# Optimization experiments

Hardware: AMD Instinct MI355X
Metric: run time of the kernel (lower is better)

Reference implementation:

```python
import jax, jax.numpy as jnp
import numpy as np

N = 50000        # nodes
E = 1_600_000    # edges
IN = 64          # in_channels
HID = 16         # hidden_dim (per-head channels)
HEADS = 8
OUT = 32         # out_channels
B = 256          # graphs in batch
NEG_SLOPE = 0.2  # PyG GATv2Conv default


def gatv2_conv(x, edge_index, wl, bl, wr, br, att, bias, heads, ch, concat, num_nodes):
    """Faithful GATv2Conv (PyG semantics, eval mode, add self-loops disabled upstream
    is not the case in PyG default, but the module uses default add_self_loops=True;
    we add them here)."""
    src, dst = edge_index[0], edge_index[1]
    # PyG default add_self_loops=True
    loop = jnp.arange(num_nodes, dtype=src.dtype)
    src = jnp.concatenate([src, loop])
    dst = jnp.concatenate([dst, loop])
    xl = (x @ wl + bl).reshape(num_nodes, heads, ch)  # source transform
    xr = (x @ wr + br).reshape(num_nodes, heads, ch)  # target transform
    # per-edge GATv2 score: att . leaky_relu(xl[src] + xr[dst])
    e = jax.nn.leaky_relu(xl[src] + xr[dst], NEG_SLOPE)          # [E, H, C]
    logits = jnp.einsum('ehc,hc->eh', e, att)                     # [E, H]
    # segment softmax over incoming edges of each dst node (max detached, as in PyG)
    m = jax.lax.stop_gradient(jax.ops.segment_max(logits, dst, num_segments=num_nodes))
    a = jnp.exp(logits - m[dst])
    denom = jax.ops.segment_sum(a, dst, num_segments=num_nodes)
    alpha = a / (denom[dst] + 1e-16)                              # [E, H]
    msg = xl[src] * alpha[..., None]                              # [E, H, C]
    out = jax.ops.segment_sum(msg, dst, num_segments=num_nodes)   # [N, H, C]
    if concat:
        out = out.reshape(num_nodes, heads * ch) + bias
    else:
        out = out.mean(axis=1) + bias
    return out


def global_mean_pool(x, batch, num_graphs):
    s = jax.ops.segment_sum(x, batch, num_segments=num_graphs)
    cnt = jax.ops.segment_sum(jnp.ones((x.shape[0],), x.dtype), batch, num_segments=num_graphs)
    return s / jnp.maximum(cnt, 1.0)[:, None]


def setup_inputs() -> dict:
    key = jax.random.key(0)
    ks = jax.random.split(key, 24)
    f32 = jnp.float32
    def g(k, shape, s=0.1):
        return jax.random.normal(k, shape, f32) * s
    inp = {
        'x': jax.random.normal(ks[0], (N, IN), f32),
        'edge_index': jax.random.randint(ks[1], (2, E), 0, N, dtype=jnp.int32),
        'batch': jnp.sort(jax.random.randint(ks[2], (N,), 0, B, dtype=jnp.int32)),
        # conv1: GATv2Conv(IN -> HID, heads=HEADS, concat=True)
        'wl1': g(ks[3], (IN, HEADS * HID)), 'bl1': jnp.zeros((HEADS * HID,), f32),
        'wr1': g(ks[4], (IN, HEADS * HID)), 'br1': jnp.zeros((HEADS * HID,), f32),
        'att1': g(ks[5], (HEADS, HID)),
        'bias1': jnp.zeros((HEADS * HID,), f32),
        # conv2: GATv2Conv(HEADS*HID -> HID, heads=1, concat=False)
        'wl2': g(ks[6], (HEADS * HID, HID)), 'bl2': jnp.zeros((HID,), f32),
        'wr2': g(ks[7], (HEADS * HID, HID)), 'br2': jnp.zeros((HID,), f32),
        'att2': g(ks[8], (1, HID)),
        'bias2': jnp.zeros((HID,), f32),
        # MLP: HID -> 2*HID -> HID -> OUT
        'w_m1': g(ks[9], (HID, 2 * HID)), 'b_m1': jnp.zeros((2 * HID,), f32),
        'w_m2': g(ks[10], (2 * HID, HID)), 'b_m2': jnp.zeros((HID,), f32),
        'w_m3': g(ks[11], (HID, OUT)), 'b_m3': jnp.zeros((OUT,), f32),
    }
    return inp


def reference(x, edge_index, batch,
              wl1, bl1, wr1, br1, att1, bias1,
              wl2, bl2, wr2, br2, att2, bias2,
              w_m1, b_m1, w_m2, b_m2, w_m3, b_m3):
    # eval mode: all dropouts are identity
    h = jax.nn.elu(gatv2_conv(x, edge_index, wl1, bl1, wr1, br1, att1, bias1,
                              HEADS, HID, True, N))
    h = jax.nn.elu(gatv2_conv(h, edge_index, wl2, bl2, wr2, br2, att2, bias2,
                              1, HID, False, N))
    h = global_mean_pool(h, batch, B)                 # [B, HID]
    h = jax.nn.elu(h @ w_m1 + b_m1)
    h = jax.nn.elu(h @ w_m2 + b_m2)
    return h @ w_m3 + b_m3                            # [B, OUT]
```

## Files before the change

### kernel.cpp

```cpp
#include <hip/hip_runtime.h>
#include <hip/hip_bf16.h>
#include <hip/hip_fp16.h>
#include <math.h>

#define NN   50000
#define NE   1600000
#define EP   (NE + NN)
#define NB   256
#define BK_SH 6
#define BKN  (1 << BK_SH)
#define NBKT ((NN + BKN - 1) >> BK_SH)
#define CAP_SH 12
#define CAP  (1 << CAP_SH)
#define ET   8
#define EB   (256 * ET)
#define EBLK ((NE + EB - 1) / EB)
#define G1   ((NN + 31) / 32)

__device__ __forceinline__ float elu_f(float x)   { return x > 0.0f ? x : expm1f(x); }
__device__ __forceinline__ float lrelu_f(float x) { return fmaxf(x, 0.2f * x); }

typedef _Float16 f16x2 __attribute__((ext_vector_type(2)));

__global__ __launch_bounds__(256) void k_gemm1_bucket(
    const float* __restrict__ x, const float* __restrict__ wl,
    const float* __restrict__ bl, const float* __restrict__ wr,
    const float* __restrict__ br, __half* __restrict__ xl1, float* __restrict__ xr1,
    const int* __restrict__ ei, int* __restrict__ bcursor,
    unsigned int* __restrict__ bb)
{
    __shared__ float xs[32 * 64];
    __shared__ int lh[NBKT];
    __shared__ int cur[NBKT];
    const int tid = threadIdx.x;

    if (blockIdx.x < G1) {
        const int n0  = blockIdx.x * 32;
        const int nrem = min(32, NN - n0);

        const float4* xg = (const float4*)(x + (size_t)n0 * 64);
        float4* xs4 = (float4*)xs;
        const int lim4 = nrem * 16;
        for (int i = tid; i < lim4; i += 256) xs4[i] = xg[i];
        __syncthreads();

        const int g  = tid >> 6;
        const int c0 = (tid & 63) * 4;
        const bool isl = (c0 < 128);
        const float* w  = isl ? wl : wr;
        const float* b  = isl ? bl : br;
        const int    cw = isl ? c0 : (c0 - 128);

        float4 acc[8];
#pragma unroll
        for (int r = 0; r < 8; ++r) acc[r] = make_float4(0.f, 0.f, 0.f, 0.f);

        for (int k4 = 0; k4 < 16; ++k4) {
            const float4 w0 = *(const float4*)&w[(k4*4+0)*128 + cw];
            const float4 w1 = *(const float4*)&w[(k4*4+1)*128 + cw];
            const float4 w2 = *(const float4*)&w[(k4*4+2)*128 + cw];
            const float4 w3 = *(const float4*)&w[(k4*4+3)*128 + cw];
#pragma unroll
            for (int r = 0; r < 8; ++r) {
                const float4 xv = xs4[(g*8+r)*16 + k4];
                acc[r].x += xv.x*w0.x + xv.y*w1.x + xv.z*w2.x + xv.w*w3.x;
                acc[r].y += xv.x*w0.y + xv.y*w1.y + xv.z*w2.y + xv.w*w3.y;
                acc[r].z += xv.x*w0.z + xv.y*w1.z + xv.z*w2.z + xv.w*w3.z;
                acc[r].w += xv.x*w0.w + xv.y*w1.w + xv.z*w2.w + xv.w*w3.w;
            }
        }
        const float4 bv = *(const float4*)&b[cw];
#pragma unroll
        for (int r = 0; r < 8; ++r) {
            const int row = g*8 + r;
            if (row < nrem) {
                float4 o = make_float4(acc[r].x + bv.x, acc[r].y + bv.y,
                                       acc[r].z + bv.z, acc[r].w + bv.w);
                if (isl) {
                    __half2* dst = (__half2*)&xl1[(size_t)(n0 + row) * 128 + cw];
                    dst[0] = __floats2half2_rn(o.x, o.y);
                    dst[1] = __floats2half2_rn(o.z, o.w);
                } else {
                    *(float4*)&xr1[(size_t)(n0 + row) * 128 + cw] = o;
                }
            }
        }
    } else {
        const int bid = blockIdx.x - G1;
        for (int i = tid; i < NBKT; i += 256) lh[i] = 0;
        __syncthreads();

        const int t = bid * 256 + tid;
        const bool act = (t * ET < NE);
        int4 dreg[ET / 4];
        if (act) {
            const int4* dp = (const int4*)&ei[NE + t * ET];
#pragma unroll
            for (int q = 0; q < ET / 4; ++q) {
                dreg[q] = dp[q];
                atomicAdd(&lh[dreg[q].x >> BK_SH], 1);
                atomicAdd(&lh[dreg[q].y >> BK_SH], 1);
                atomicAdd(&lh[dreg[q].z >> BK_SH], 1);
                atomicAdd(&lh[dreg[q].w >> BK_SH], 1);
            }
        }
        __syncthreads();
        for (int i = tid; i < NBKT; i += 256) {
            int h = lh[i];
            if (h > 0) cur[i] = (i << CAP_SH) + atomicAdd(&bcursor[i], h);
        }
        __syncthreads();
        if (act) {
            const int4* sp = (const int4*)&ei[t * ET];
#pragma unroll
            for (int q = 0; q < ET / 4; ++q) {
                int4 s = sp[q];
                int4 d = dreg[q];
                int bkt, p;
                bkt = d.x >> BK_SH; p = atomicAdd(&cur[bkt], 1);
                if (p < ((bkt + 1) << CAP_SH))
                    bb[p] = ((unsigned)(d.x & (BKN-1)) << 17) | (unsigned)s.x;
                bkt = d.y >> BK_SH; p = atomicAdd(&cur[bkt], 1);
                if (p < ((bkt + 1) << CAP_SH))
                    bb[p] = ((unsigned)(d.y & (BKN-1)) << 17) | (unsigned)s.y;
                bkt = d.z >> BK_SH; p = atomicAdd(&cur[bkt], 1);
                if (p < ((bkt + 1) << CAP_SH))
                    bb[p] = ((unsigned)(d.z & (BKN-1)) << 17) | (unsigned)s.z;
                bkt = d.w >> BK_SH; p = atomicAdd(&cur[bkt], 1);
                if (p < ((bkt + 1) << CAP_SH))
                    bb[p] = ((unsigned)(d.w & (BKN-1)) << 17) | (unsigned)s.w;
            }
        }
    }
}

__global__ __launch_bounds__(256) void k_bfinal(
    const unsigned int* __restrict__ bb, const int* __restrict__ bcursor,
    int* __restrict__ rowp, int* __restrict__ slist)
{
    __shared__ int cnt[BKN], cur[BKN];
    __shared__ int red[256];
    const int b = blockIdx.x, tid = threadIdx.x;
    const int db0 = b << BK_SH;
    const int dn  = min(BKN, NN - db0);

    int part = 0;
    for (int i = tid; i < b; i += 256)
        part += min(bcursor[i], CAP);
    red[tid] = part;
    __syncthreads();
    for (int ofs = 128; ofs >= 1; ofs >>= 1) {
        if (tid < ofs) red[tid] += red[tid + ofs];
        __syncthreads();
    }
    const int ebeg = red[0];
    const int count = min(bcursor[b], CAP);
    const unsigned int* src = bb + ((size_t)b << CAP_SH);
    const int out0 = ebeg + db0;

    int c0 = 0;
    if (tid < BKN) {
        c0 = (tid < dn) ? 1 : 0;
        cnt[tid] = c0;
    }
    __syncthreads();
    for (int i = tid; i < count; i += 256)
        atomicAdd(&cnt[src[i] >> 17], 1);
    __syncthreads();
    if (tid < BKN) c0 = cnt[tid];
    for (int ofs = 1; ofs < BKN; ofs <<= 1) {
        int v = 0;
        if (tid < BKN && tid >= ofs) v = cnt[tid - ofs];
        __syncthreads();
        if (tid < BKN) cnt[tid] += v;
        __syncthreads();
    }
    if (tid < BKN) {
        int ex = cnt[tid] - c0;
        cur[tid] = ex + 1;
        if (tid < dn) {
            rowp[db0 + tid] = out0 + ex;
            slist[out0 + ex] = db0 + tid;
        }
    }
    if (b == 0 && tid == 0) rowp[NN] = EP;
    __syncthreads();
    for (int i = tid; i < count; i += 256) {
        unsigned u = src[i];
        int p = atomicAdd(&cur[u >> 17], 1);
        slist[out0 + p] = (int)(u & 0x1FFFFu);
    }
}

__global__ __launch_bounds__(256) void k_conv1_agg(
    const __half* __restrict__ xl1, const float* __restrict__ xr1,
    const float* __restrict__ att, const float* __restrict__ bias1,
    const int* __restrict__ rowp, const int* __restrict__ slist,
    const float* __restrict__ wl2, const float* __restrict__ bl2,
    const float* __restrict__ wr2, const float* __restrict__ br2,
    __half* __restrict__ xl2, float* __restrict__ xr2)
{
    __shared__ float wcombt[32 * 132];
    __shared__ float bcomb[32];
    __shared__ float h1rows[4 * 128];
    const int tid = threadIdx.x;

    for (int i = tid; i < 2048; i += 256) {
        const int cc = i >> 4, jj = i & 15;
        wcombt[jj * 132 + cc]        = wl2[i];
        wcombt[(16 + jj) * 132 + cc] = wr2[i];
    }
    if (tid < 16) { bcomb[tid] = bl2[tid]; bcomb[16 + tid] = br2[tid]; }

    const int d = (blockIdx.x * 256 + tid) >> 6;
    const int lane = tid & 63;
    const int h = lane >> 3, e = lane & 7;
    const int cb = h * 16;

    f16x2 xrh[8], ath[8];
    {
        const float4* xrp = (const float4*)&xr1[(size_t)d * 128 + cb];
        const float4* atp = (const float4*)&att[cb];
#pragma unroll
        for (int q = 0; q < 4; ++q) {
            float4 a4 = xrp[q];
            xrh[2*q]   = (f16x2){(_Float16)a4.x, (_Float16)a4.y};
            xrh[2*q+1] = (f16x2){(_Float16)a4.z, (_Float16)a4.w};
            float4 b4 = atp[q];
            ath[2*q]   = (f16x2){(_Float16)b4.x, (_Float16)b4.y};
            ath[2*q+1] = (f16x2){(_Float16)b4.z, (_Float16)b4.w};
        }
    }
    const f16x2 c02 = {(_Float16)0.2f, (_Float16)0.2f};

    const int beg = rowp[d], end = rowp[d + 1];

    float den = 0.f;
    float a[16];
#pragma unroll
    for (int c = 0; c < 16; ++c) a[c] = 0.f;

    for (int base = beg; base < end; base += 64) {
        const int nb = min(64, end - base);
        int sv = (lane < nb) ? slist[base + lane] : 0;
        for (int c8 = 0; c8 * 8 < nb; c8 += 2) {
            const int idx0 = c8 * 8 + e;
            const int idx1 = idx0 + 8;
            const int s0 = __shfl(sv, idx0);
            const int s1 = __shfl(sv, idx1 & 63);
            const bool e0 = (idx0 < nb), e1 = (idx1 < nb);
            float4 p0, p1, q0, q1;
            if (e0) {
                const float4* vp = (const float4*)(xl1 + (size_t)s0 * 128 + cb);
                p0 = vp[0]; p1 = vp[1];
            }
            if (e1) {
                const float4* vp = (const float4*)(xl1 + (size_t)s1 * 128 + cb);
                q0 = vp[0]; q1 = vp[1];
            }
            if (e0) {
                const f16x2* hh = (const f16x2*)&p0;
                const f16x2* hg = (const f16x2*)&p1;
                float s = 0.f;
#pragma unroll
                for (int q = 0; q < 4; ++q) {
                    f16x2 t = hh[q] + xrh[q];
                    t = __builtin_elementwise_max(t, t * c02);
                    s = __builtin_amdgcn_fdot2(ath[q], t, s, false);
                }
#pragma unroll
                for (int q = 0; q < 4; ++q) {
                    f16x2 t = hg[q] + xrh[4+q];
                    t = __builtin_elementwise_max(t, t * c02);
                    s = __builtin_amdgcn_fdot2(ath[4+q], t, s, false);
                }
                const float w = __expf(fminf(s, 80.f));
                den += w;
#pragma unroll
                for (int q = 0; q < 4; ++q) {
                    a[2*q]     += w * (float)hh[q].x;
                    a[2*q+1]   += w * (float)hh[q].y;
                    a[8+2*q]   += w * (float)hg[q].x;
                    a[8+2*q+1] += w * (float)hg[q].y;
                }
            }
            if (e1) {
                const f16x2* hh = (const f16x2*)&q0;
                const f16x2* hg = (const f16x2*)&q1;
                float s = 0.f;
#pragma unroll
                for (int q = 0; q < 4; ++q) {
                    f16x2 t = hh[q] + xrh[q];
                    t = __builtin_elementwise_max(t, t * c02);
                    s = __builtin_amdgcn_fdot2(ath[q], t, s, false);
                }
#pragma unroll
                for (int q = 0; q < 4; ++q) {
                    f16x2 t = hg[q] + xrh[4+q];
                    t = __builtin_elementwise_max(t, t * c02);
                    s = __builtin_amdgcn_fdot2(ath[4+q], t, s, false);
                }
                const float w = __expf(fminf(s, 80.f));
                den += w;
#pragma unroll
                for (int q = 0; q < 4; ++q) {
                    a[2*q]     += w * (float)hh[q].x;
                    a[2*q+1]   += w * (float)hh[q].y;
                    a[8+2*q]   += w * (float)hg[q].x;
                    a[8+2*q+1] += w * (float)hg[q].y;
                }
            }
        }
    }

    den += __shfl_xor(den, 1);
    den += __shfl_xor(den, 2);
    den += __shfl_xor(den, 4);

    const bool b0 = (e & 1), b1 = (e & 2), b2 = (e & 4);
    float t1[8], u1[8];
#pragma unroll
    for (int j = 0; j < 8; ++j) {
        t1[j] = b0 ? a[j + 8] : a[j];
        u1[j] = b0 ? a[j] : a[j + 8];
    }
#pragma unroll
    for (int j = 0; j < 8; ++j) t1[j] += __shfl_xor(u1[j], 1);
    float t2[4], u2[4];
#pragma unroll
    for (int j = 0; j < 4; ++j) {
        t2[j] = b1 ? t1[j + 4] : t1[j];
        u2[j] = b1 ? t1[j] : t1[j + 4];
    }
#pragma unroll
    for (int j = 0; j < 4; ++j) t2[j] += __shfl_xor(u2[j], 2);
    float t3[2], u3[2];
#pragma unroll
    for (int j = 0; j < 2; ++j) {
        t3[j] = b2 ? t2[j + 2] : t2[j];
        u3[j] = b2 ? t2[j] : t2[j + 2];
    }
#pragma unroll
    for (int j = 0; j < 2; ++j) t3[j] += __shfl_xor(u3[j], 4);

    const int c0 = (b0 ? 8 : 0) + (b1 ? 4 : 0) + (b2 ? 2 : 0);
    const float inv = 1.0f / (den + 1e-16f);
    const int c = cb + c0;
    const float o0 = elu_f(t3[0] * inv + bias1[c]);
    const float o1 = elu_f(t3[1] * inv + bias1[c + 1]);

    const int wv = tid >> 6;
    *(float2*)&h1rows[wv * 128 + c] = make_float2(o0, o1);
    __syncthreads();
    {
        const int j = lane & 31;
        const int half = lane >> 5;
        const float* hr = &h1rows[wv * 128 + half * 64];
        const float* wc = &wcombt[j * 132 + half * 64];
        float sum = 0.f;
#pragma unroll
        for (int cc = 0; cc < 64; cc += 4) {
            const float4 hv = *(const float4*)&hr[cc];
            const float4 wv4 = *(const float4*)&wc[cc];
            sum += hv.x*wv4.x + hv.y*wv4.y + hv.z*wv4.z + hv.w*wv4.w;
        }
        sum += __shfl_xor(sum, 32);
        if (half == 0) {
            sum += bcomb[j];
            if (j < 16) xl2[(size_t)d * 16 + j] = __float2half(sum);
            else        xr2[(size_t)d * 16 + (j - 16)] = sum;
        }
    }
}

__global__ __launch_bounds__(256) void k_conv2_agg(
    const __half* __restrict__ xl2, const float* __restrict__ xr2,
    const float* __restrict__ att, const float* __restrict__ bias2,
    const int* __restrict__ rowp, const int* __restrict__ slist,
    float* __restrict__ h2)
{
    const int d = (blockIdx.x * 256 + threadIdx.x) >> 6;
    if (d >= NN) return;
    const int lane = threadIdx.x & 63;

    f16x2 xrh[8], ath[8];
    {
        const float4* xrp = (const float4*)&xr2[(size_t)d * 16];
        const float4* atp = (const float4*)&att[0];
#pragma unroll
        for (int q = 0; q < 4; ++q) {
            float4 a4 = xrp[q];
            xrh[2*q]   = (f16x2){(_Float16)a4.x, (_Float16)a4.y};
            xrh[2*q+1] = (f16x2){(_Float16)a4.z, (_Float16)a4.w};
            float4 b4 = atp[q];
            ath[2*q]   = (f16x2){(_Float16)b4.x, (_Float16)b4.y};
            ath[2*q+1] = (f16x2){(_Float16)b4.z, (_Float16)b4.w};
        }
    }
    const f16x2 c02 = {(_Float16)0.2f, (_Float16)0.2f};

    const int beg = rowp[d];
    const int total = rowp[d + 1] - beg;

    float den = 0.f;
    float a[16];
#pragma unroll
    for (int c = 0; c < 16; ++c) a[c] = 0.f;

    for (int j = lane; j < total; j += 64) {
        const int src = slist[beg + j];
        const float4* vp = (const float4*)(xl2 + (size_t)src * 16);
        const float4 r0 = vp[0], r1 = vp[1];
        const f16x2* hh = (const f16x2*)&r0;
        const f16x2* hg = (const f16x2*)&r1;
        float s = 0.f;
#pragma unroll
        for (int q = 0; q < 4; ++q) {
            f16x2 t = hh[q] + xrh[q];
            t = __builtin_elementwise_max(t, t * c02);
            s = __builtin_amdgcn_fdot2(ath[q], t, s, false);
        }
#pragma unroll
        for (int q = 0; q < 4; ++q) {
            f16x2 t = hg[q] + xrh[4+q];
            t = __builtin_elementwise_max(t, t * c02);
            s = __builtin_amdgcn_fdot2(ath[4+q], t, s, false);
        }
        const float w = __expf(fminf(s, 80.f));
        den += w;
#pragma unroll
        for (int q = 0; q < 4; ++q) {
            a[2*q]     += w * (float)hh[q].x;
            a[2*q+1]   += w * (float)hh[q].y;
            a[8+2*q]   += w * (float)hg[q].x;
            a[8+2*q+1] += w * (float)hg[q].y;
        }
    }

    den += __shfl_xor(den, 1);
    den += __shfl_xor(den, 2);
    den += __shfl_xor(den, 4);
    den += __shfl_xor(den, 8);
    den += __shfl_xor(den, 16);
    den += __shfl_xor(den, 32);

    const bool b0 = (lane & 1), b1 = (lane & 2), b2 = (lane & 4), b3 = (lane & 8);
    float t1[8], u1[8];
#pragma unroll
    for (int j = 0; j < 8; ++j) {
        t1[j] = b0 ? a[j + 8] : a[j];
        u1[j] = b0 ? a[j] : a[j + 8];
    }
#pragma unroll
    for (int j = 0; j < 8; ++j) t1[j] += __shfl_xor(u1[j], 1);
    float t2[4], u2[4];
#pragma unroll
    for (int j = 0; j < 4; ++j) {
        t2[j] = b1 ? t1[j + 4] : t1[j];
        u2[j] = b1 ? t1[j] : t1[j + 4];
    }
#pragma unroll
    for (int j = 0; j < 4; ++j) t2[j] += __shfl_xor(u2[j], 2);
    float t3[2], u3[2];
#pragma unroll
    for (int j = 0; j < 2; ++j) {
        t3[j] = b2 ? t2[j + 2] : t2[j];
        u3[j] = b2 ? t2[j] : t2[j + 2];
    }
#pragma unroll
    for (int j = 0; j < 2; ++j) t3[j] += __shfl_xor(u3[j], 4);
    float t4 = b3 ? t3[1] : t3[0];
    float u4 = b3 ? t3[0] : t3[1];
    t4 += __shfl_xor(u4, 8);
    t4 += __shfl_xor(t4, 16);
    t4 += __shfl_xor(t4, 32);

    if (lane < 16) {
        const int c = (b0 ? 8 : 0) + (b1 ? 4 : 0) + (b2 ? 2 : 0) + (b3 ? 1 : 0);
        const float inv = 1.0f / (den + 1e-16f);
        h2[(size_t)d * 16 + c] = elu_f(t4 * inv + bias2[c]);
    }
}

__global__ __launch_bounds__(256) void k_pool_mlp(
    const float* __restrict__ h2, const int* __restrict__ batch,
    const float* __restrict__ w1, const float* __restrict__ b1,
    const float* __restrict__ w2, const float* __restrict__ b2,
    const float* __restrict__ w3, const float* __restrict__ b3,
    float* __restrict__ out)
{
    __shared__ int se[2];
    __shared__ float sm[256];
    __shared__ float hb[16], t1s[32], t2s[16];
    const int b = blockIdx.x, tid = threadIdx.x;
    if (tid < 2) {
        int key = b + tid, lo = 0, hi = NN;
        while (lo < hi) {
            int mid = (lo + hi) >> 1;
            if (batch[mid] < key) lo = mid + 1; else hi = mid;
        }
        se[tid] = lo;
    }
    __syncthreads();
    const int s = se[0], e = se[1];
    const int c = tid & 15, slot = tid >> 4;
    float acc = 0.f;
    for (int n = s + slot; n < e; n += 16) acc += h2[(size_t)n * 16 + c];
    sm[tid] = acc;
    __syncthreads();
    for (int ofs = 128; ofs >= 16; ofs >>= 1) {
        if (tid < ofs) sm[tid] += sm[tid + ofs];
        __syncthreads();
    }
    if (tid < 16) hb[tid] = sm[tid] / fmaxf((float)(e - s), 1.0f);
    __syncthreads();
    if (tid < 32) {
        float v = b1[tid];
        for (int k = 0; k < 16; ++k) v += hb[k] * w1[k * 32 + tid];
        t1s[tid] = elu_f(v);
    }
    __syncthreads();
    if (tid < 16) {
        float v = b2[tid];
        for (int k = 0; k < 32; ++k) v += t1s[k] * w2[k * 16 + tid];
        t2s[tid] = elu_f(v);
    }
    __syncthreads();
    if (tid < 32) {
        float v = b3[tid];
        for (int k = 0; k < 16; ++k) v += t2s[k] * w3[k * 32 + tid];
        out[b * 32 + tid] = v;
    }
}

extern "C" void kernel_launch(void* const* d_in, const int* in_sizes, int n_in,
                              void* d_out, int out_size, void* d_ws, size_t ws_size,
                              hipStream_t stream)
{
    const float* x     = (const float*)d_in[0];
    const int*   ei    = (const int*)d_in[1];
    const int*   batch = (const int*)d_in[2];
    const float* wl1   = (const float*)d_in[3];
    const float* bl1   = (const float*)d_in[4];
    const float* wr1   = (const float*)d_in[5];
    const float* br1   = (const float*)d_in[6];
    const float* att1  = (const float*)d_in[7];
    const float* bias1 = (const float*)d_in[8];
    const float* wl2   = (const float*)d_in[9];
    const float* bl2   = (const float*)d_in[10];
    const float* wr2   = (const float*)d_in[11];
    const float* br2   = (const float*)d_in[12];
    const float* att2  = (const float*)d_in[13];
    const float* bias2 = (const float*)d_in[14];
    const float* wm1   = (const float*)d_in[15];
    const float* bm1   = (const float*)d_in[16];
    const float* wm2   = (const float*)d_in[17];
    const float* bm2   = (const float*)d_in[18];
    const float* wm3   = (const float*)d_in[19];
    const float* bm3   = (const float*)d_in[20];
    float* out = (float*)d_out;

    char* base = (char*)d_ws;
    size_t off = 0;
    auto alloc = [&](size_t bytes) -> void* {
        void* p = base + off;
        off += (bytes + 255) & ~(size_t)255;
        return p;
    };
    __half* xl1  = (__half*)alloc((size_t)NN * 128 * 2);
    float* xr1   = (float*)alloc((size_t)NN * 128 * 4);
    int*   slist = (int*)  alloc((size_t)EP * 4);
    unsigned int* bb = (unsigned int*)alloc((size_t)NBKT * CAP * 4);
    int*   rowp  = (int*)  alloc((size_t)(NN + 1) * 4);
    int*   bcursor=(int*)  alloc((size_t)NBKT * 4);
    __half* xl2  = (__half*)alloc((size_t)NN * 16 * 2);
    float* xr2   = (float*)alloc((size_t)NN * 16 * 4);
    float* h2    = (float*)alloc((size_t)NN * 16 * 4);

    (void)hipMemsetAsync(bcursor, 0, (size_t)NBKT * 4, stream);
    k_gemm1_bucket<<<G1 + EBLK, 256, 0, stream>>>(x, wl1, bl1, wr1, br1, xl1, xr1,
                                                  ei, bcursor, bb);
    k_bfinal<<<NBKT, 256, 0, stream>>>(bb, bcursor, rowp, slist);
    k_conv1_agg<<<(NN * 64) / 256, 256, 0, stream>>>(xl1, xr1, att1, bias1, rowp, slist,
                                                     wl2, bl2, wr2, br2, xl2, xr2);
    k_conv2_agg<<<(NN * 64) / 256, 256, 0, stream>>>(xl2, xr2, att2, bias2, rowp, slist, h2);
    k_pool_mlp<<<NB, 256, 0, stream>>>(h2, batch, wm1, bm1, wm2, bm2, wm3, bm3, out);
}
```

Baseline: 279.5 us.

## Fuse CSR bucket finalization into both aggregation kernels via shared-memory local CSR

Removes the separate k_bfinal kernel and the global rowp/slist arrays. Each aggregation block now handles one 64-node bucket with 512 threads, building that bucket's local row pointers and source list in LDS from the bucket buffer, then lets each of 8 waves process 8 destination nodes in turn. This saves one launch and the global CSR write and read-back. In exchange the bucket sort is done twice, once per conv kernel, and the grid is much smaller with a large LDS footprint per block, which can lower occupancy and load balance.

Result: slower. 286.9 us (+2.6%).

```diff
diff --git a/kernel.cpp b/kernel.cpp
--- a/kernel.cpp
+++ b/kernel.cpp
@@ -134,123 +134,105 @@
     }
 }
 
-__global__ __launch_bounds__(256) void k_bfinal(
-    const unsigned int* __restrict__ bb, const int* __restrict__ bcursor,
-    int* __restrict__ rowp, int* __restrict__ slist)
-{
-    __shared__ int cnt[BKN], cur[BKN];
-    __shared__ int red[256];
-    const int b = blockIdx.x, tid = threadIdx.x;
-    const int db0 = b << BK_SH;
-    const int dn  = min(BKN, NN - db0);
-
-    int part = 0;
-    for (int i = tid; i < b; i += 256)
-        part += min(bcursor[i], CAP);
-    red[tid] = part;
-    __syncthreads();
-    for (int ofs = 128; ofs >= 1; ofs >>= 1) {
-        if (tid < ofs) red[tid] += red[tid + ofs];
-        __syncthreads();
-    }
-    const int ebeg = red[0];
-    const int count = min(bcursor[b], CAP);
-    const unsigned int* src = bb + ((size_t)b << CAP_SH);
-    const int out0 = ebeg + db0;
-
-    int c0 = 0;
-    if (tid < BKN) {
-        c0 = (tid < dn) ? 1 : 0;
-        cnt[tid] = c0;
-    }
-    __syncthreads();
-    for (int i = tid; i < count; i += 256)
-        atomicAdd(&cnt[src[i] >> 17], 1);
-    __syncthreads();
-    if (tid < BKN) c0 = cnt[tid];
-    for (int ofs = 1; ofs < BKN; ofs <<= 1) {
-        int v = 0;
-        if (tid < BKN && tid >= ofs) v = cnt[tid - ofs];
-        __syncthreads();
-        if (tid < BKN) cnt[tid] += v;
-        __syncthreads();
-    }
-    if (tid < BKN) {
-        int ex = cnt[tid] - c0;
-        cur[tid] = ex + 1;
-        if (tid < dn) {
-            rowp[db0 + tid] = out0 + ex;
-            slist[out0 + ex] = db0 + tid;
-        }
-    }
-    if (b == 0 && tid == 0) rowp[NN] = EP;
-    __syncthreads();
-    for (int i = tid; i < count; i += 256) {
-        unsigned u = src[i];
-        int p = atomicAdd(&cur[u >> 17], 1);
-        slist[out0 + p] = (int)(u & 0x1FFFFu);
-    }
-}
-
-__global__ __launch_bounds__(256) void k_conv1_agg(
+__global__ __launch_bounds__(512) void k_conv1_agg(
     const __half* __restrict__ xl1, const float* __restrict__ xr1,
     const float* __restrict__ att, const float* __restrict__ bias1,
-    const int* __restrict__ rowp, const int* __restrict__ slist,
+    const unsigned int* __restrict__ bb, const int* __restrict__ bcursor,
     const float* __restrict__ wl2, const float* __restrict__ bl2,
     const float* __restrict__ wr2, const float* __restrict__ br2,
     __half* __restrict__ xl2, float* __restrict__ xr2)
 {
     __shared__ float wcombt[32 * 132];
     __shared__ float bcomb[32];
-    __shared__ float h1rows[4 * 128];
+    __shared__ float h1rows[8 * 128];
+    __shared__ int lcnt[BKN], lcur[BKN];
+    __shared__ int lrowp[BKN + 1];
+    __shared__ int lsl[CAP + BKN];
     const int tid = threadIdx.x;
-
-    for (int i = tid; i < 2048; i += 256) {
+    const int b = blockIdx.x;
+    const int db0 = b << BK_SH;
+    const int dn  = min(BKN, NN - db0);
+    const int count = min(bcursor[b], CAP);
+    const unsigned int* src = bb + ((size_t)b << CAP_SH);
+
+    for (int i = tid; i < 2048; i += 512) {
         const int cc = i >> 4, jj = i & 15;
         wcombt[jj * 132 + cc]        = wl2[i];
         wcombt[(16 + jj) * 132 + cc] = wr2[i];
     }
     if (tid < 16) { bcomb[tid] = bl2[tid]; bcomb[16 + tid] = br2[tid]; }
 
-    const int d = (blockIdx.x * 256 + tid) >> 6;
-    const int lane = tid & 63;
+    int selfc = 0;
+    if (tid < BKN) {
+        selfc = (tid < dn) ? 1 : 0;
+        lcnt[tid] = selfc;
+    }
+    __syncthreads();
+    for (int i = tid; i < count; i += 512)
+        atomicAdd(&lcnt[src[i] >> 17], 1);
+    __syncthreads();
+    int orig = 0;
+    if (tid < BKN) orig = lcnt[tid];
+    for (int ofs = 1; ofs < BKN; ofs <<= 1) {
+        int v = 0;
+        if (tid < BKN && tid >= ofs) v = lcnt[tid - ofs];
+        __syncthreads();
+        if (tid < BKN) lcnt[tid] += v;
+        __syncthreads();
+    }
+    if (tid < BKN) {
+        const int ex = lcnt[tid] - orig;
+        lrowp[tid] = ex;
+        lcur[tid] = ex + 1;
+        if (tid < dn) lsl[ex] = db0 + tid;
+        if (tid == BKN - 1) lrowp[BKN] = lcnt[tid];
+    }
+    __syncthreads();
+    for (int i = tid; i < count; i += 512) {
+        const unsigned u = src[i];
+        const int p = atomicAdd(&lcur[u >> 17], 1);
+        lsl[p] = (int)(u & 0x1FFFFu);
+    }
+    __syncthreads();
+
+    const int wv = tid >> 6, lane = tid & 63;
     const int h = lane >> 3, e = lane & 7;
     const int cb = h * 16;
-
-    f16x2 xrh[8], ath[8];
-    {
-        const float4* xrp = (const float4*)&xr1[(size_t)d * 128 + cb];
-        const float4* atp = (const float4*)&att[cb];
-#pragma unroll
-        for (int q = 0; q < 4; ++q) {
-            float4 a4 = xrp[q];
-            xrh[2*q]   = (f16x2){(_Float16)a4.x, (_Float16)a4.y};
-            xrh[2*q+1] = (f16x2){(_Float16)a4.z, (_Float16)a4.w};
-            float4 b4 = atp[q];
-            ath[2*q]   = (f16x2){(_Float16)b4.x, (_Float16)b4.y};
-            ath[2*q+1] = (f16x2){(_Float16)b4.z, (_Float16)b4.w};
-        }
-    }
     const f16x2 c02 = {(_Float16)0.2f, (_Float16)0.2f};
 
-    const int beg = rowp[d], end = rowp[d + 1];
-
-    float den = 0.f;
-    float a[16];
-#pragma unroll
-    for (int c = 0; c < 16; ++c) a[c] = 0.f;
-
-    for (int base = beg; base < end; base += 64) {
-        const int nb = min(64, end - base);
-        int sv = (lane < nb) ? slist[base + lane] : 0;
-        for (int c8 = 0; c8 * 8 < nb; c8 += 2) {
-            const int idx0 = c8 * 8 + e;
-            const int idx1 = idx0 + 8;
-            const int s0 = __shfl(sv, idx0);
-            const int s1 = __shfl(sv, idx1 & 63);
-            const bool e0 = (idx0 < nb), e1 = (idx1 < nb);
+    for (int di = 0; di < 8; ++di) {
+        const int dloc = wv * 8 + di;
+        if (dloc >= dn) break;
+        const int d = db0 + dloc;
+
+        f16x2 xrh[8], ath[8];
+        {
+            const float4* xrp = (const float4*)&xr1[(size_t)d * 128 + cb];
+            const float4* atp = (const float4*)&att[cb];
+#pragma unroll
+            for (int q = 0; q < 4; ++q) {
+                float4 a4 = xrp[q];
+                xrh[2*q]   = (f16x2){(_Float16)a4.x, (_Float16)a4.y};
+                xrh[2*q+1] = (f16x2){(_Float16)a4.z, (_Float16)a4.w};
+                float4 b4 = atp[q];
+                ath[2*q]   = (f16x2){(_Float16)b4.x, (_Float16)b4.y};
+                ath[2*q+1] = (f16x2){(_Float16)b4.z, (_Float16)b4.w};
+            }
+        }
+        const int beg = lrowp[dloc];
+        const int deg = lrowp[dloc + 1] - beg;
+
+        float den = 0.f;
+        float a[16];
+#pragma unroll
+        for (int c = 0; c < 16; ++c) a[c] = 0.f;
+
+        for (int idx0 = e; idx0 < deg; idx0 += 16) {
+            const int s0 = lsl[beg + idx0];
+            const bool e1 = (idx0 + 8 < deg);
+            const int s1 = e1 ? lsl[beg + idx0 + 8] : 0;
             float4 p0, p1, q0, q1;
-            if (e0) {
+            {
                 const float4* vp = (const float4*)(xl1 + (size_t)s0 * 128 + cb);
                 p0 = vp[0]; p1 = vp[1];
             }
@@ -258,7 +240,7 @@
                 const float4* vp = (const float4*)(xl1 + (size_t)s1 * 128 + cb);
                 q0 = vp[0]; q1 = vp[1];
             }
-            if (e0) {
+            {
                 const f16x2* hh = (const f16x2*)&p0;
                 const f16x2* hg = (const f16x2*)&p1;
                 float s = 0.f;
@@ -311,174 +293,218 @@
                 }
             }
         }
-    }
-
-    den += __shfl_xor(den, 1);
-    den += __shfl_xor(den, 2);
-    den += __shfl_xor(den, 4);
-
-    const bool b0 = (e & 1), b1 = (e & 2), b2 = (e & 4);
-    float t1[8], u1[8];
-#pragma unroll
-    for (int j = 0; j < 8; ++j) {
-        t1[j] = b0 ? a[j + 8] : a[j];
-        u1[j] = b0 ? a[j] : a[j + 8];
-    }
-#pragma unroll
-    for (int j = 0; j < 8; ++j) t1[j] += __shfl_xor(u1[j], 1);
-    float t2[4], u2[4];
-#pragma unroll
-    for (int j = 0; j < 4; ++j) {
-        t2[j] = b1 ? t1[j + 4] : t1[j];
-        u2[j] = b1 ? t1[j] : t1[j + 4];
-    }
-#pragma unroll
-    for (int j = 0; j < 4; ++j) t2[j] += __shfl_xor(u2[j], 2);
-    float t3[2], u3[2];
-#pragma unroll
-    for (int j = 0; j < 2; ++j) {
-        t3[j] = b2 ? t2[j + 2] : t2[j];
-        u3[j] = b2 ? t2[j] : t2[j + 2];
-    }
-#pragma unroll
-    for (int j = 0; j < 2; ++j) t3[j] += __shfl_xor(u3[j], 4);
-
-    const int c0 = (b0 ? 8 : 0) + (b1 ? 4 : 0) + (b2 ? 2 : 0);
-    const float inv = 1.0f / (den + 1e-16f);
-    const int c = cb + c0;
-    const float o0 = elu_f(t3[0] * inv + bias1[c]);
-    const float o1 = elu_f(t3[1] * inv + bias1[c + 1]);
-
-    const int wv = tid >> 6;
-    *(float2*)&h1rows[wv * 128 + c] = make_float2(o0, o1);
-    __syncthreads();
-    {
-        const int j = lane & 31;
-        const int half = lane >> 5;
-        const float* hr = &h1rows[wv * 128 + half * 64];
-        const float* wc = &wcombt[j * 132 + half * 64];
-        float sum = 0.f;
-#pragma unroll
-        for (int cc = 0; cc < 64; cc += 4) {
-            const float4 hv = *(const float4*)&hr[cc];
-            const float4 wv4 = *(const float4*)&wc[cc];
-            sum += hv.x*wv4.x + hv.y*wv4.y + hv.z*wv4.z + hv.w*wv4.w;
-        }
-        sum += __shfl_xor(sum, 32);
-        if (half == 0) {
-            sum += bcomb[j];
-            if (j < 16) xl2[(size_t)d * 16 + j] = __float2half(sum);
-            else        xr2[(size_t)d * 16 + (j - 16)] = sum;
+
+        den += __shfl_xor(den, 1);
+        den += __shfl_xor(den, 2);
+        den += __shfl_xor(den, 4);
+
+        const bool b0 = (e & 1), b1 = (e & 2), b2 = (e & 4);
+        float t1[8], u1[8];
+#pragma unroll
+        for (int j = 0; j < 8; ++j) {
+            t1[j] = b0 ? a[j + 8] : a[j];
+            u1[j] = b0 ? a[j] : a[j + 8];
+        }
+#pragma unroll
+        for (int j = 0; j < 8; ++j) t1[j] += __shfl_xor(u1[j], 1);
+        float t2[4], u2[4];
+#pragma unroll
+        for (int j = 0; j < 4; ++j) {
+            t2[j] = b1 ? t1[j + 4] : t1[j];
+            u2[j] = b1 ? t1[j] : t1[j + 4];
+        }
+#pragma unroll
+        for (int j = 0; j < 4; ++j) t2[j] += __shfl_xor(u2[j], 2);
+        float t3[2], u3[2];
+#pragma unroll
+        for (int j = 0; j < 2; ++j) {
+            t3[j] = b2 ? t2[j + 2] : t2[j];
+            u3[j] = b2 ? t2[j] : t2[j + 2];
+        }
+#pragma unroll
+        for (int j = 0; j < 2; ++j) t3[j] += __shfl_xor(u3[j], 4);
+
+        const int c0 = (b0 ? 8 : 0) + (b1 ? 4 : 0) + (b2 ? 2 : 0);
+        const float inv = 1.0f / (den + 1e-16f);
+        const int c = cb + c0;
+        const float o0 = elu_f(t3[0] * inv + bias1[c]);
+        const float o1 = elu_f(t3[1] * inv + bias1[c + 1]);
+
+        *(float2*)&h1rows[wv * 128 + c] = make_float2(o0, o1);
+        {
+            const int j = lane & 31;
+            const int half = lane >> 5;
+            const float* hr = &h1rows[wv * 128 + half * 64];
+            const float* wc = &wcombt[j * 132 + half * 64];
+            float sum = 0.f;
+#pragma unroll
+            for (int cc = 0; cc < 64; cc += 4) {
+                const float4 hv = *(const float4*)&hr[cc];
+                const float4 wv4 = *(const float4*)&wc[cc];
+                sum += hv.x*wv4.x + hv.y*wv4.y + hv.z*wv4.z + hv.w*wv4.w;
+            }
+            sum += __shfl_xor(sum, 32);
+            if (half == 0) {
+                sum += bcomb[j];
+                if (j < 16) xl2[(size_t)d * 16 + j] = __float2half(sum);
+                else        xr2[(size_t)d * 16 + (j - 16)] = sum;
+            }
         }
     }
 }
 
-__global__ __launch_bounds__(256) void k_conv2_agg(
+__global__ __launch_bounds__(512) void k_conv2_agg(
     const __half* __restrict__ xl2, const float* __restrict__ xr2,
     const float* __restrict__ att, const float* __restrict__ bias2,
-    const int* __restrict__ rowp, const int* __restrict__ slist,
+    const unsigned int* __restrict__ bb, const int* __restrict__ bcursor,
     float* __restrict__ h2)
 {
-    const int d = (blockIdx.x * 256 + threadIdx.x) >> 6;
-    if (d >= NN) return;
-    const int lane = threadIdx.x & 63;
-
-    f16x2 xrh[8], ath[8];
-    {
-        const float4* xrp = (const float4*)&xr2[(size_t)d * 16];
-        const float4* atp = (const float4*)&att[0];
-#pragma unroll
-        for (int q = 0; q < 4; ++q) {
-            float4 a4 = xrp[q];
-            xrh[2*q]   = (f16x2){(_Float16)a4.x, (_Float16)a4.y};
-            xrh[2*q+1] = (f16x2){(_Float16)a4.z, (_Float16)a4.w};
-            float4 b4 = atp[q];
-            ath[2*q]   = (f16x2){(_Float16)b4.x, (_Float16)b4.y};
-            ath[2*q+1] = (f16x2){(_Float16)b4.z, (_Float16)b4.w};
-        }
-    }
+    __shared__ int lcnt[BKN], lcur[BKN];
+    __shared__ int lrowp[BKN + 1];
+    __shared__ int lsl[CAP + BKN];
+    const int tid = threadIdx.x;
+    const int b = blockIdx.x;
+    const int db0 = b << BK_SH;
+    const int dn  = min(BKN, NN - db0);
+    const int count = min(bcursor[b], CAP);
+    const unsigned int* src = bb + ((size_t)b << CAP_SH);
+
+    int selfc = 0;
+    if (tid < BKN) {
+        selfc = (tid < dn) ? 1 : 0;
+        lcnt[tid] = selfc;
+    }
+    __syncthreads();
+    for (int i = tid; i < count; i += 512)
+        atomicAdd(&lcnt[src[i] >> 17], 1);
+    __syncthreads();
+    int orig = 0;
+    if (tid < BKN) orig = lcnt[tid];
+    for (int ofs = 1; ofs < BKN; ofs <<= 1) {
+        int v = 0;
+        if (tid < BKN && tid >= ofs) v = lcnt[tid - ofs];
+        __syncthreads();
+        if (tid < BKN) lcnt[tid] += v;
+        __syncthreads();
+    }
+    if (tid < BKN) {
+        const int ex = lcnt[tid] - orig;
+        lrowp[tid] = ex;
+        lcur[tid] = ex + 1;
+        if (tid < dn) lsl[ex] = db0 + tid;
+        if (tid == BKN - 1) lrowp[BKN] = lcnt[tid];
+    }
+    __syncthreads();
+    for (int i = tid; i < count; i += 512) {
+        const unsigned u = src[i];
+        const int p = atomicAdd(&lcur[u >> 17], 1);
+        lsl[p] = (int)(u & 0x1FFFFu);
+    }
+    __syncthreads();
+
+    const int wv = tid >> 6, lane = tid & 63;
     const f16x2 c02 = {(_Float16)0.2f, (_Float16)0.2f};
 
-    const int beg = rowp[d];
-    const int total = rowp[d + 1] - beg;
-
-    float den = 0.f;
-    float a[16];
-#pragma unroll
-    for (int c = 0; c < 16; ++c) a[c] = 0.f;
-
-    for (int j = lane; j < total; j += 64) {
-        const int src = slist[beg + j];
-        const float4* vp = (const float4*)(xl2 + (size_t)src * 16);
-        const float4 r0 = vp[0], r1 = vp[1];
-        const f16x2* hh = (const f16x2*)&r0;
-        const f16x2* hg = (const f16x2*)&r1;
-        float s = 0.f;
-#pragma unroll
-        for (int q = 0; q < 4; ++q) {
-            f16x2 t = hh[q] + xrh[q];
-            t = __builtin_elementwise_max(t, t * c02);
-            s = __builtin_amdgcn_fdot2(ath[q], t, s, false);
-        }
-#pragma unroll
-        for (int q = 0; q < 4; ++q) {
-            f16x2 t = hg[q] + xrh[4+q];
-            t = __builtin_elementwise_max(t, t * c02);
-            s = __builtin_amdgcn_fdot2(ath[4+q], t, s, false);
-        }
-        const float w = __expf(fminf(s, 80.f));
-        den += w;
-#pragma unroll
-        for (int q = 0; q < 4; ++q) {
-            a[2*q]     += w * (float)hh[q].x;
-            a[2*q+1]   += w * (float)hh[q].y;
-            a[8+2*q]   += w * (float)hg[q].x;
-            a[8+2*q+1] += w * (float)hg[q].y;
-        }
-    }
-
-    den += __shfl_xor(den, 1);
-    den += __shfl_xor(den, 2);
-    den += __shfl_xor(den, 4);
-    den += __shfl_xor(den, 8);
-    den += __shfl_xor(den, 16);
-    den += __shfl_xor(den, 32);
-
-    const bool b0 = (lane & 1), b1 = (lane & 2), b2 = (lane & 4), b3 = (lane & 8);
-    float t1[8], u1[8];
-#pragma unroll
-    for (int j = 0; j < 8; ++j) {
-        t1[j] = b0 ? a[j + 8] : a[j];
-        u1[j] = b0 ? a[j] : a[j + 8];
-    }
-#pragma unroll
-    for (int j = 0; j < 8; ++j) t1[j] += __shfl_xor(u1[j], 1);
-    float t2[4], u2[4];
-#pragma unroll
-    for (int j = 0; j < 4; ++j) {
-        t2[j] = b1 ? t1[j + 4] : t1[j];
-        u2[j] = b1 ? t1[j] : t1[j + 4];
-    }
-#pragma unroll
-    for (int j = 0; j < 4; ++j) t2[j] += __shfl_xor(u2[j], 2);
-    float t3[2], u3[2];
-#pragma unroll
-    for (int j = 0; j < 2; ++j) {
-        t3[j] = b2 ? t2[j + 2] : t2[j];
-        u3[j] = b2 ? t2[j] : t2[j + 2];
-    }
-#pragma unroll
-    for (int j = 0; j < 2; ++j) t3[j] += __shfl_xor(u3[j], 4);
-    float t4 = b3 ? t3[1] : t3[0];
-    float u4 = b3 ? t3[0] : t3[1];
-    t4 += __shfl_xor(u4, 8);
-    t4 += __shfl_xor(t4, 16);
-    t4 += __shfl_xor(t4, 32);
-
-    if (lane < 16) {
-        const int c = (b0 ? 8 : 0) + (b1 ? 4 : 0) + (b2 ? 2 : 0) + (b3 ? 1 : 0);
-        const float inv = 1.0f / (den + 1e-16f);
-        h2[(size_t)d * 16 + c] = elu_f(t4 * inv + bias2[c]);
+    for (int di = 0; di < 8; ++di) {
+        const int dloc = wv * 8 + di;
+        if (dloc >= dn) break;
+        const int d = db0 + dloc;
+
+        f16x2 xrh[8], ath[8];
+        {
+            const float4* xrp = (const float4*)&xr2[(size_t)d * 16];
+            const float4* atp = (const float4*)&att[0];
+#pragma unroll
+            for (int q = 0; q < 4; ++q) {
+                float4 a4 = xrp[q];
+                xrh[2*q]   = (f16x2){(_Float16)a4.x, (_Float16)a4.y};
+                xrh[2*q+1] = (f16x2){(_Float16)a4.z, (_Float16)a4.w};
+                float4 b4 = atp[q];
+                ath[2*q]   = (f16x2){(_Float16)b4.x, (_Float16)b4.y};
+                ath[2*q+1] = (f16x2){(_Float16)b4.z, (_Float16)b4.w};
+            }
+        }
+        const int beg = lrowp[dloc];
+        const int deg = lrowp[dloc + 1] - beg;
+
+        float den = 0.f;
+        float a[16];
+#pragma unroll
+        for (int c = 0; c < 16; ++c) a[c] = 0.f;
+
+        for (int j = lane; j < deg; j += 64) {
+            const int s0 = lsl[beg + j];
+            const float4* vp = (const float4*)(xl2 + (size_t)s0 * 16);
+            const float4 r0 = vp[0], r1 = vp[1];
+            const f16x2* hh = (const f16x2*)&r0;
+            const f16x2* hg = (const f16x2*)&r1;
+            float s = 0.f;
+#pragma unroll
+            for (int q = 0; q < 4; ++q) {
+                f16x2 t = hh[q] + xrh[q];
+                t = __builtin_elementwise_max(t, t * c02);
+                s = __builtin_amdgcn_fdot2(ath[q], t, s, false);
+            }
+#pragma unroll
+            for (int q = 0; q < 4; ++q) {
+                f16x2 t = hg[q] + xrh[4+q];
+                t = __builtin_elementwise_max(t, t * c02);
+                s = __builtin_amdgcn_fdot2(ath[4+q], t, s, false);
+            }
+            const float w = __expf(fminf(s, 80.f));
+            den += w;
+#pragma unroll
+            for (int q = 0; q < 4; ++q) {
+                a[2*q]     += w * (float)hh[q].x;
+                a[2*q+1]   += w * (float)hh[q].y;
+                a[8+2*q]   += w * (float)hg[q].x;
+                a[8+2*q+1] += w * (float)hg[q].y;
+            }
+        }
+
+        den += __shfl_xor(den, 1);
+        den += __shfl_xor(den, 2);
+        den += __shfl_xor(den, 4);
+        den += __shfl_xor(den, 8);
+        den += __shfl_xor(den, 16);
+        den += __shfl_xor(den, 32);
+
+        const bool b0 = (lane & 1), b1 = (lane & 2), b2 = (lane & 4), b3 = (lane & 8);
+        float t1[8], u1[8];
+#pragma unroll
+        for (int j = 0; j < 8; ++j) {
+            t1[j] = b0 ? a[j + 8] : a[j];
+            u1[j] = b0 ? a[j] : a[j + 8];
+        }
+#pragma unroll
+        for (int j = 0; j < 8; ++j) t1[j] += __shfl_xor(u1[j], 1);
+        float t2[4], u2[4];
+#pragma unroll
+        for (int j = 0; j < 4; ++j) {
+            t2[j] = b1 ? t1[j + 4] : t1[j];
+            u2[j] = b1 ? t1[j] : t1[j + 4];
+        }
+#pragma unroll
+        for (int j = 0; j < 4; ++j) t2[j] += __shfl_xor(u2[j], 2);
+        float t3[2], u3[2];
+#pragma unroll
+        for (int j = 0; j < 2; ++j) {
+            t3[j] = b2 ? t2[j + 2] : t2[j];
+            u3[j] = b2 ? t2[j] : t2[j + 2];
+        }
+#pragma unroll
+        for (int j = 0; j < 2; ++j) t3[j] += __shfl_xor(u3[j], 4);
+        float t4 = b3 ? t3[1] : t3[0];
+        float u4 = b3 ? t3[0] : t3[1];
+        t4 += __shfl_xor(u4, 8);
+        t4 += __shfl_xor(t4, 16);
+        t4 += __shfl_xor(t4, 32);
+
+        if (lane < 16) {
+            const int c = (b0 ? 8 : 0) + (b1 ? 4 : 0) + (b2 ? 2 : 0) + (b3 ? 1 : 0);
+            const float inv = 1.0f / (den + 1e-16f);
+            h2[(size_t)d * 16 + c] = elu_f(t4 * inv + bias2[c]);
+        }
     }
 }
 
@@ -569,9 +595,7 @@
     };
     __half* xl1  = (__half*)alloc((size_t)NN * 128 * 2);
     float* xr1   = (float*)alloc((size_t)NN * 128 * 4);
-    int*   slist = (int*)  alloc((size_t)EP * 4);
     unsigned int* bb = (unsigned int*)alloc((size_t)NBKT * CAP * 4);
-    int*   rowp  = (int*)  alloc((size_t)(NN + 1) * 4);
     int*   bcursor=(int*)  alloc((size_t)NBKT * 4);
     __half* xl2  = (__half*)alloc((size_t)NN * 16 * 2);
     float* xr2   = (float*)alloc((size_t)NN * 16 * 4);
@@ -580,9 +604,8 @@
     (void)hipMemsetAsync(bcursor, 0, (size_t)NBKT * 4, stream);
     k_gemm1_bucket<<<G1 + EBLK, 256, 0, stream>>>(x, wl1, bl1, wr1, br1, xl1, xr1,
                                                   ei, bcursor, bb);
-    k_bfinal<<<NBKT, 256, 0, stream>>>(bb, bcursor, rowp, slist);
-    k_conv1_agg<<<(NN * 64) / 256, 256, 0, stream>>>(xl1, xr1, att1, bias1, rowp, slist,
-                                                     wl2, bl2, wr2, br2, xl2, xr2);
-    k_conv2_agg<<<(NN * 64) / 256, 256, 0, stream>>>(xl2, xr2, att2, bias2, rowp, slist, h2);
+    k_conv1_agg<<<NBKT, 512, 0, stream>>>(xl1, xr1, att1, bias1, bb, bcursor,
+                                          wl2, bl2, wr2, br2, xl2, xr2);
+    k_conv2_agg<<<NBKT, 512, 0, stream>>>(xl2, xr2, att2, bias2, bb, bcursor, h2);
     k_pool_mlp<<<NB, 256, 0, stream>>>(h2, batch, wm1, bm1, wm2, bm2, wm3, bm3, out);
 }
```
